# Optimization experiments

Hardware: AMD Instinct MI355X
Metric: run time of the kernel (lower is better)

## Reference

```python
import jax, jax.numpy as jnp
import numpy as np

N, T = 2048, 128
E, H = 128, 256
V, L = 30000, 1000


def setup_inputs() -> dict:
    key = jax.random.key(0)
    ks = jax.random.split(key, 10)
    tokens = jax.random.randint(ks[0], (N, T), 0, V)
    lengths = jax.random.randint(ks[1], (N,), 1, T + 1)  # each seq has >=1 valid step
    labels = jax.random.randint(ks[2], (N,), 0, L)
    s_e = 1.0 / np.sqrt(H)
    emb = jax.random.normal(ks[3], (V, E), dtype=jnp.float32)
    W_ih = jax.random.uniform(ks[4], (4 * H, E), minval=-s_e, maxval=s_e, dtype=jnp.float32)
    W_hh = jax.random.uniform(ks[5], (4 * H, H), minval=-s_e, maxval=s_e, dtype=jnp.float32)
    b_ih = jax.random.uniform(ks[6], (4 * H,), minval=-s_e, maxval=s_e, dtype=jnp.float32)
    b_hh = jax.random.uniform(ks[7], (4 * H,), minval=-s_e, maxval=s_e, dtype=jnp.float32)
    s_h = 1.0 / np.sqrt(H)
    W_out = jax.random.uniform(ks[8], (L, H), minval=-s_h, maxval=s_h, dtype=jnp.float32)
    b_out = jax.random.uniform(ks[9], (L,), minval=-s_h, maxval=s_h, dtype=jnp.float32)
    return {"tokens": tokens, "lengths": lengths, "labels": labels, "emb": emb,
            "W_ih": W_ih, "W_hh": W_hh, "b_ih": b_ih, "b_hh": b_hh,
            "W_out": W_out, "b_out": b_out}


def _lstm_final(tokens, lengths, emb, W_ih, W_hh, b_ih, b_hh):
    # Batched ragged LSTM: freeze state once t >= length (matches per-seq loop).
    x = emb[tokens]                                    # [N,T,E]
    xg = jnp.einsum('nte,ge->ntg', x, W_ih) + b_ih     # [N,T,4H] precomputed input gates
    xg_t = jnp.transpose(xg, (1, 0, 2))                # [T,N,4H]
    mask_t = (jnp.arange(T)[:, None] < lengths[None, :])  # [T,N]
    h0 = jnp.zeros((tokens.shape[0], H), jnp.float32)
    c0 = jnp.zeros_like(h0)

    def step(carry, inp):
        h, c = carry
        xgt, m = inp
        gates = xgt + h @ W_hh.T + b_hh                # [N,4H]
        i, f, g, o = jnp.split(gates, 4, axis=-1)
        i = jax.nn.sigmoid(i); f = jax.nn.sigmoid(f)
        g = jnp.tanh(g); o = jax.nn.sigmoid(o)
        c_new = f * c + i * g
        h_new = o * jnp.tanh(c_new)
        mm = m[:, None]
        return (jnp.where(mm, h_new, h), jnp.where(mm, c_new, c)), None

    (h_f, c_f), _ = jax.lax.scan(step, (h0, c0), (xg_t, mask_t))
    return h_f, c_f                                    # final valid h, c per sequence


def reference(tokens, lengths, labels, emb, W_ih, W_hh, b_ih, b_hh, W_out, b_out):
    h_f, c_f = _lstm_final(tokens, lengths, emb, W_ih, W_hh, b_ih, b_hh)
    logits = h_f @ W_out.T + b_out                     # [N,L]
    logp = jax.nn.log_softmax(logits, axis=-1)
    # NLLLoss per sequence, summed then divided by count -> mean
    loss = -jnp.mean(logp[jnp.arange(logp.shape[0]), labels])
    embeds = jnp.mean(c_f, axis=0)                     # mean of final cell states, [H]
    return embeds, loss
```

## Files before the change

### kernel.cpp

```cpp
#include <hip/hip_runtime.h>
#include <hip/hip_bf16.h>
#include <math.h>

#define NSEQ 2048
#define TT   128
#define EE   128
#define HH   256
#define GG   1024
#define LL   1000
#define NT   512
#define NGRP 32
#define NMEM 8
#define SEQG 64
#define NKT  12
#define NMT  64
#define NKT_O 8
#define WSA_ELEMS (NMT * NKT * 64 * 8)
#define WSO_ELEMS (NMT * NKT_O * 64 * 8)
#define GHF_SHORTS ((size_t)NGRP * NMEM * 2 * 4 * 64 * 8)

typedef __attribute__((ext_vector_type(8))) short bf16x8;
typedef __attribute__((ext_vector_type(4))) float f32x4;
typedef unsigned long long u64;

__device__ __forceinline__ unsigned short f2bf(float f) {
    union { float f; unsigned u; } v; v.f = f;
    unsigned r = v.u + 0x7FFF + ((v.u >> 16) & 1);
    return (unsigned short)(r >> 16);
}
__device__ __forceinline__ float sigf(float x) { return 1.0f / (1.0f + __expf(-x)); }
__device__ __forceinline__ float tanh_fast(float x) { return 1.0f - 2.0f / (1.0f + __expf(2.0f * x)); }

__device__ __forceinline__ void st8_sys(unsigned short* p, unsigned lo, unsigned hi) {
    u64 v = (u64)lo | ((u64)hi << 32);
    __hip_atomic_store((u64*)p, v, __ATOMIC_RELAXED, __HIP_MEMORY_SCOPE_SYSTEM);
}
__device__ __forceinline__ bf16x8 ld16_sys(const unsigned short* p) {
    u64 lo = __hip_atomic_load((const u64*)p,       __ATOMIC_RELAXED, __HIP_MEMORY_SCOPE_SYSTEM);
    u64 hi = __hip_atomic_load((const u64*)(p + 4), __ATOMIC_RELAXED, __HIP_MEMORY_SCOPE_SYSTEM);
    union { u64 q[2]; bf16x8 v; } u; u.q[0] = lo; u.q[1] = hi;
    return u.v;
}

__global__ void init_out_kernel(float* out, int* flags) {
    int i = blockIdx.x * blockDim.x + threadIdx.x;
    if (i < HH + 1) out[i] = 0.0f;
    if (i < NGRP * NMEM) flags[i] = 0;
}

__global__ void convert_weights(const float* __restrict__ Wih, const float* __restrict__ Whh,
                                const float* __restrict__ Wout,
                                unsigned short* __restrict__ wsA, unsigned short* __restrict__ wsO) {
    int gid = blockIdx.x * blockDim.x + threadIdx.x;
    if (gid < NMT * NKT * 64) {
        int lane = gid & 63, tile = gid >> 6;
        int kt = tile % NKT, mt = tile / NKT;
        int row = mt * 16 + (lane & 15);
        int kb  = kt * 32 + (lane >> 4) * 8;
        unsigned short o[8];
#pragma unroll
        for (int j = 0; j < 8; ++j) {
            int k = kb + j;
            float v = (k < EE) ? Wih[row * EE + k] : Whh[row * HH + (k - EE)];
            o[j] = f2bf(v);
        }
        uint4 pk;
        pk.x = o[0] | ((unsigned)o[1] << 16); pk.y = o[2] | ((unsigned)o[3] << 16);
        pk.z = o[4] | ((unsigned)o[5] << 16); pk.w = o[6] | ((unsigned)o[7] << 16);
        *(uint4*)(wsA + (size_t)gid * 8) = pk;
    } else {
        int g2 = gid - NMT * NKT * 64;
        if (g2 < NMT * NKT_O * 64) {
            int lane = g2 & 63, tile = g2 >> 6;
            int kt = tile % NKT_O, mt = tile / NKT_O;
            int row = mt * 16 + (lane & 15);
            int ub  = kt * 32 + (lane >> 4) * 8;
            unsigned short o[8];
#pragma unroll
            for (int j = 0; j < 8; ++j)
                o[j] = (row < LL) ? f2bf(Wout[row * HH + ub + j]) : (unsigned short)0;
            uint4 pk;
            pk.x = o[0] | ((unsigned)o[1] << 16); pk.y = o[2] | ((unsigned)o[3] << 16);
            pk.z = o[4] | ((unsigned)o[5] << 16); pk.w = o[6] | ((unsigned)o[7] << 16);
            *(uint4*)(wsO + (size_t)g2 * 8) = pk;
        }
    }
}

__launch_bounds__(NT, 2)
__global__ void lstm_group_kernel(
    const int* __restrict__ tokens, const int* __restrict__ lengths,
    const int* __restrict__ labels, const float* __restrict__ emb,
    const float* __restrict__ bih,  const float* __restrict__ bhh,
    const float* __restrict__ bout,
    const unsigned short* __restrict__ wsA, const unsigned short* __restrict__ wsO,
    unsigned short* __restrict__ ghf, int* __restrict__ flags,
    float* __restrict__ out)
{
    __shared__ __align__(16) unsigned short wlds[8 * 12 * 64 * 8];
    __shared__ __align__(16) unsigned short xf[2 * 4 * 4 * 64 * 8];
    __shared__ __align__(16) unsigned short hf[2 * 4 * 64 * 8];
    __shared__ float bias_s[128];
    __shared__ int   labv[SEQG];
    __shared__ int   ready_s;

    const int tid = threadIdx.x;
    const int w   = tid >> 6;
    const int l   = tid & 63;
    const int lq  = l >> 4;
    const int ls  = l & 15;
    const int jj  = w >> 2;
    const int cg  = w & 3;
    const int grp = blockIdx.x & (NGRP - 1);
    const int m   = blockIdx.x >> 5;
    const int n0  = grp * SEQG;

    int* const flagBase = flags + grp * NMEM;

    int maxlen = lengths[n0 + l];
#pragma unroll
    for (int s = 1; s < 64; s <<= 1) maxlen = max(maxlen, __shfl_xor(maxlen, s, 64));
    const int len_s = lengths[n0 + cg * 16 + ls];

    if (tid < SEQG) labv[tid] = labels[n0 + tid];
    if (tid < 128) {
        int g = tid >> 5, u = tid & 31;
        int row = 256 * g + 32 * m + u;
        bias_s[tid] = bih[row] + bhh[row];
    }
    if (tid == 0) ready_s = 0;

    for (int idx = tid; idx < 8 * 12 * 64; idx += NT) {
        int mtl = idx / 768;
        int rem = idx - mtl * 768;
        int kt = rem >> 6, l2 = rem & 63;
        int g = mtl >> 1, j2 = mtl & 1;
        int gmt = 16 * g + 2 * m + j2;
        *(uint4*)&wlds[(size_t)idx * 8] =
            *(const uint4*)(wsA + ((size_t)(gmt * NKT + kt) * 64 + l2) * 8);
    }

    if (tid < 256) {
        uint4 z = {0, 0, 0, 0};
        *(uint4*)&hf[(size_t)tid * 8] = z;
        size_t base = ((size_t)((grp * NMEM + m) * 2 + 0) * 4) * 512 + (size_t)tid * 8;
        st8_sys(&ghf[base], 0, 0);
        st8_sys(&ghf[base + 4], 0, 0);
    }

    const int xs_s   = tid & 63;
    const int xs_oct = tid >> 6;

    {
        int tok = tokens[(n0 + xs_s) * TT + 0];
        const float* er = emb + (size_t)tok * EE + 16 * xs_oct;
#pragma unroll
        for (int dc = 0; dc < 4; ++dc) {
            f32x4 xv = *(const f32x4*)(er + 4 * dc);
            int d0 = 16 * xs_oct + 4 * dc;
            int kt = d0 >> 5, cgs = xs_s >> 4;
            int lanep = (xs_s & 15) + 16 * ((d0 >> 3) & 3);
            uint2 pk;
            pk.x = f2bf(xv[0]) | ((unsigned)f2bf(xv[1]) << 16);
            pk.y = f2bf(xv[2]) | ((unsigned)f2bf(xv[3]) << 16);
            *(uint2*)&xf[(size_t)(((0 * 4 + kt) * 4 + cgs) * 64 + lanep) * 8 + (d0 & 4)] = pk;
        }
    }
    __syncthreads();
    if (tid == 0)
        __hip_atomic_store(&flagBase[m], 1, __ATOMIC_RELAXED, __HIP_MEMORY_SCOPE_SYSTEM);

    auto relay_wait = [&](int need) {
        if (w == 0) {
            int f;
            do {
                f = 0x7fffffff;
                if (l < NMEM)
                    f = __hip_atomic_load(&flagBase[l], __ATOMIC_RELAXED, __HIP_MEMORY_SCOPE_SYSTEM);
                f = min(f, __shfl_xor(f, 1, 64));
                f = min(f, __shfl_xor(f, 2, 64));
                f = min(f, __shfl_xor(f, 4, 64));
                f = __shfl(f, 0, 64);
                if (f < need) __builtin_amdgcn_s_sleep(2);
            } while (f < need);
            __hip_atomic_store(&ready_s, need, __ATOMIC_RELEASE, __HIP_MEMORY_SCOPE_WORKGROUP);
        } else {
            while (__hip_atomic_load(&ready_s, __ATOMIC_ACQUIRE, __HIP_MEMORY_SCOPE_WORKGROUP) < need)
                __builtin_amdgcn_s_sleep(1);
        }
    };

    float c_reg[4], h_reg[4];
#pragma unroll
    for (int r = 0; r < 4; ++r) { c_reg[r] = 0.0f; h_reg[r] = 0.0f; }

    const int u8      = 2 * jj + (lq >> 1);
    const int lanep_h = 16 * u8 + ls;
    const int joff_h  = 4 * (lq & 1);
    const size_t gb0  = ((size_t)((grp * NMEM + m) * 2 + 0) * 4 + cg) * 512 + (size_t)lanep_h * 8 + joff_h;
    const size_t gb1  = gb0 + 4 * 512;

    for (int t = 0; t < maxlen; ++t) {
        const int cur = t & 1, nxt = cur ^ 1;

        bf16x8 bx[4];
#pragma unroll
        for (int kt = 0; kt < 4; ++kt)
            bx[kt] = *(const bf16x8*)&xf[(size_t)(((cur * 4 + kt) * 4 + cg) * 64 + l) * 8];
        const bf16x8 bo = *(const bf16x8*)&hf[(size_t)((cur * 4 + cg) * 64 + l) * 8];

        const bool doX = (t + 1 < maxlen);
        f32x4 xv[4];
        if (doX) {
            int tok = tokens[(n0 + xs_s) * TT + t + 1];
            const float* er = emb + (size_t)tok * EE + 16 * xs_oct;
#pragma unroll
            for (int dc = 0; dc < 4; ++dc) xv[dc] = *(const f32x4*)(er + 4 * dc);
        }

        f32x4 acc[4];
#pragma unroll
        for (int g = 0; g < 4; ++g)
            acc[g] = *(const f32x4*)&bias_s[g * 32 + 16 * jj + 4 * lq];

#pragma unroll
        for (int kt = 0; kt < 4; ++kt)
#pragma unroll
            for (int g = 0; g < 4; ++g)
                acc[g] = __builtin_amdgcn_mfma_f32_16x16x32_bf16(
                    *(const bf16x8*)&wlds[(size_t)(((2 * g + jj) * 12 + kt) * 64 + l) * 8],
                    bx[kt], acc[g], 0, 0, 0);

        relay_wait(t + 1);

        bf16x8 bp[7];
#pragma unroll
        for (int i = 0; i < 7; ++i) {
            int p = i + (i >= m ? 1 : 0);
            size_t b = ((size_t)((grp * NMEM + p) * 2 + cur) * 4 + cg) * 512;
            bp[i] = ld16_sys(&ghf[b + (size_t)l * 8]);
        }

#pragma unroll
        for (int g = 0; g < 4; ++g)
            acc[g] = __builtin_amdgcn_mfma_f32_16x16x32_bf16(
                *(const bf16x8*)&wlds[(size_t)(((2 * g + jj) * 12 + 4 + m) * 64 + l) * 8],
                bo, acc[g], 0, 0, 0);
#pragma unroll
        for (int i = 0; i < 7; ++i) {
            int p = i + (i >= m ? 1 : 0);
            int kt = 4 + p;
#pragma unroll
            for (int g = 0; g < 4; ++g)
                acc[g] = __builtin_amdgcn_mfma_f32_16x16x32_bf16(
                    *(const bf16x8*)&wlds[(size_t)(((2 * g + jj) * 12 + kt) * 64 + l) * 8],
                    bp[i], acc[g], 0, 0, 0);
        }

        const bool live = (t < len_s);
#pragma unroll
        for (int r = 0; r < 4; ++r) {
            if (live) {
                float ig = sigf(acc[0][r]);
                float fg = sigf(acc[1][r]);
                float gg = tanh_fast(acc[2][r]);
                float og = sigf(acc[3][r]);
                float cc = fg * c_reg[r] + ig * gg;
                c_reg[r] = cc;
                h_reg[r] = og * tanh_fast(cc);
            }
        }

        {
            uint2 hp;
            hp.x = f2bf(h_reg[0]) | ((unsigned)f2bf(h_reg[1]) << 16);
            hp.y = f2bf(h_reg[2]) | ((unsigned)f2bf(h_reg[3]) << 16);
            *(uint2*)&hf[(size_t)((nxt * 4 + cg) * 64 + lanep_h) * 8 + joff_h] = hp;
            st8_sys(&ghf[((t + 1) & 1) ? gb1 : gb0], hp.x, hp.y);
        }
        if (doX) {
#pragma unroll
            for (int dc = 0; dc < 4; ++dc) {
                int d0 = 16 * xs_oct + 4 * dc;
                int kt = d0 >> 5, cgs = xs_s >> 4;
                int lanep = (xs_s & 15) + 16 * ((d0 >> 3) & 3);
                uint2 pk;
                pk.x = f2bf(xv[dc][0]) | ((unsigned)f2bf(xv[dc][1]) << 16);
                pk.y = f2bf(xv[dc][2]) | ((unsigned)f2bf(xv[dc][3]) << 16);
                *(uint2*)&xf[(size_t)(((nxt * 4 + kt) * 4 + cgs) * 64 + lanep) * 8 + (d0 & 4)] = pk;
            }
        }

        __syncthreads();
        if (tid == 0)
            __hip_atomic_store(&flagBase[m], t + 2, __ATOMIC_RELAXED, __HIP_MEMORY_SCOPE_SYSTEM);
    }

#pragma unroll
    for (int r = 0; r < 4; ++r) {
        float v = c_reg[r];
        v += __shfl_xor(v, 1, 64);
        v += __shfl_xor(v, 2, 64);
        v += __shfl_xor(v, 4, 64);
        v += __shfl_xor(v, 8, 64);
        if (ls == 0)
            atomicAdd(&out[32 * m + 16 * jj + 4 * lq + r], v * (1.0f / NSEQ));
    }

    if (m == 0) {
        relay_wait(maxlen + 1);
        const int fin = maxlen & 1;
        float* lg = (float*)wlds;
        float lossAcc = 0.0f;

        for (int cgo = 0; cgo < 4; ++cgo) {
            bf16x8 bq[8];
#pragma unroll
            for (int p = 0; p < 8; ++p) {
                size_t b = ((size_t)((grp * NMEM + p) * 2 + fin) * 4 + cgo) * 512;
                bq[p] = ld16_sys(&ghf[b + (size_t)l * 8]);
            }
            __syncthreads();
#pragma unroll
            for (int i = 0; i < 8; ++i) {
                int mt = 8 * w + i;
                f32x4 a = {0.0f, 0.0f, 0.0f, 0.0f};
#pragma unroll
                for (int p = 0; p < 8; ++p)
                    a = __builtin_amdgcn_mfma_f32_16x16x32_bf16(
                        *(const bf16x8*)(wsO + ((size_t)(mt * NKT_O + p) * 64 + l) * 8),
                        bq[p], a, 0, 0, 0);
#pragma unroll
                for (int r = 0; r < 4; ++r) {
                    int cls = 16 * mt + 4 * lq + r;
                    lg[(size_t)ls * 1024 + cls] = (cls < LL) ? (a[r] + bout[cls]) : -INFINITY;
                }
            }
            __syncthreads();
            const int s2 = tid >> 5;
            const int i2 = tid & 31;
            const float* row = &lg[(size_t)s2 * 1024];
            float mx = -INFINITY;
#pragma unroll
            for (int k = 0; k < 32; ++k) mx = fmaxf(mx, row[i2 + 32 * k]);
            mx = fmaxf(mx, __shfl_xor(mx, 1, 64));
            mx = fmaxf(mx, __shfl_xor(mx, 2, 64));
            mx = fmaxf(mx, __shfl_xor(mx, 4, 64));
            mx = fmaxf(mx, __shfl_xor(mx, 8, 64));
            mx = fmaxf(mx, __shfl_xor(mx, 16, 64));
            float sm = 0.0f;
#pragma unroll
            for (int k = 0; k < 32; ++k) sm += __expf(row[i2 + 32 * k] - mx);
            sm += __shfl_xor(sm, 1, 64);
            sm += __shfl_xor(sm, 2, 64);
            sm += __shfl_xor(sm, 4, 64);
            sm += __shfl_xor(sm, 8, 64);
            sm += __shfl_xor(sm, 16, 64);
            if (i2 == 0) {
                int lab = labv[cgo * 16 + s2];
                float lp = row[lab] - mx - __logf(sm);
                lossAcc += -lp;
            }
        }
        if ((tid & 31) == 0)
            atomicAdd(&out[HH], lossAcc * (1.0f / NSEQ));
    }
}

extern "C" void kernel_launch(void* const* d_in, const int* in_sizes, int n_in,
                              void* d_out, int out_size, void* d_ws, size_t ws_size,
                              hipStream_t stream)
{
    const int*   tokens  = (const int*)d_in[0];
    const int*   lengths = (const int*)d_in[1];
    const int*   labels  = (const int*)d_in[2];
    const float* emb     = (const float*)d_in[3];
    const float* Wih     = (const float*)d_in[4];
    const float* Whh     = (const float*)d_in[5];
    const float* bih     = (const float*)d_in[6];
    const float* bhh     = (const float*)d_in[7];
    const float* Wout    = (const float*)d_in[8];
    const float* bout    = (const float*)d_in[9];
    float* out = (float*)d_out;

    unsigned short* wsA  = (unsigned short*)d_ws;
    unsigned short* wsO  = wsA + WSA_ELEMS;
    unsigned short* ghf  = wsO + WSO_ELEMS;
    int*            flg  = (int*)(ghf + GHF_SHORTS);

    hipLaunchKernelGGL(init_out_kernel, dim3(1), dim3(512), 0, stream, out, flg);
    {
        int nthr = NMT * NKT * 64 + NMT * NKT_O * 64;
        hipLaunchKernelGGL(convert_weights, dim3((nthr + 255) / 256), dim3(256), 0, stream,
                           Wih, Whh, Wout, wsA, wsO);
    }
    hipLaunchKernelGGL(lstm_group_kernel, dim3(NGRP * NMEM), dim3(NT), 0, stream,
                       tokens, lengths, labels, emb, bih, bhh, bout, wsA, wsO, ghf, flg, out);
}
```

Measured before the change: 708.8 us.

## Software-pipeline input-gate MFMAs one step ahead and keep bias in registers

Computes the input-projection MFMAs for step t+1 into a separate accumulator while waiting for the cross-block relay at step t. The embedding gather moves two steps ahead, and the x staging buffer is reduced to a single buffer. Bias values now live in registers instead of LDS. This takes the input-gate MFMAs off the critical path after the relay wait, at the cost of an extra __syncthreads per step and more register pressure (accN, prefetched xv).

```diff
diff --git a/kernel.cpp b/kernel.cpp
--- a/kernel.cpp
+++ b/kernel.cpp
@@ -98,9 +98,10 @@
     float* __restrict__ out)
 {
     __shared__ __align__(16) unsigned short wlds[8 * 12 * 64 * 8];
-    __shared__ __align__(16) unsigned short xf[2 * 4 * 4 * 64 * 8];
+    __shared__ __align__(16) unsigned short xfS[4 * 4 * 64 * 8];
     __shared__ __align__(16) unsigned short hf[2 * 4 * 64 * 8];
-    __shared__ float bias_s[128];
+    __shared__ float redm[8][16];
+    __shared__ float reds[8][16];
     __shared__ int   labv[SEQG];
     __shared__ int   ready_s;
 
@@ -123,12 +124,16 @@
     const int len_s = lengths[n0 + cg * 16 + ls];
 
     if (tid < SEQG) labv[tid] = labels[n0 + tid];
-    if (tid < 128) {
-        int g = tid >> 5, u = tid & 31;
-        int row = 256 * g + 32 * m + u;
-        bias_s[tid] = bih[row] + bhh[row];
-    }
     if (tid == 0) ready_s = 0;
+
+    f32x4 biasv[4];
+#pragma unroll
+    for (int g = 0; g < 4; ++g)
+#pragma unroll
+        for (int r = 0; r < 4; ++r) {
+            int row = 256 * g + 32 * m + 16 * jj + 4 * lq + r;
+            biasv[g][r] = bih[row] + bhh[row];
+        }
 
     for (int idx = tid; idx < 8 * 12 * 64; idx += NT) {
         int mtl = idx / 768;
@@ -151,24 +156,52 @@
     const int xs_s   = tid & 63;
     const int xs_oct = tid >> 6;
 
-    {
-        int tok = tokens[(n0 + xs_s) * TT + 0];
-        const float* er = emb + (size_t)tok * EE + 16 * xs_oct;
+    auto stageX = [&](const f32x4* xv) {
 #pragma unroll
         for (int dc = 0; dc < 4; ++dc) {
-            f32x4 xv = *(const f32x4*)(er + 4 * dc);
             int d0 = 16 * xs_oct + 4 * dc;
             int kt = d0 >> 5, cgs = xs_s >> 4;
             int lanep = (xs_s & 15) + 16 * ((d0 >> 3) & 3);
             uint2 pk;
-            pk.x = f2bf(xv[0]) | ((unsigned)f2bf(xv[1]) << 16);
-            pk.y = f2bf(xv[2]) | ((unsigned)f2bf(xv[3]) << 16);
-            *(uint2*)&xf[(size_t)(((0 * 4 + kt) * 4 + cgs) * 64 + lanep) * 8 + (d0 & 4)] = pk;
-        }
+            pk.x = f2bf(xv[dc][0]) | ((unsigned)f2bf(xv[dc][1]) << 16);
+            pk.y = f2bf(xv[dc][2]) | ((unsigned)f2bf(xv[dc][3]) << 16);
+            *(uint2*)&xfS[(size_t)((kt * 4 + cgs) * 64 + lanep) * 8 + (d0 & 4)] = pk;
+        }
+    };
+
+    {
+        int tok = tokens[(n0 + xs_s) * TT + 0];
+        const float* er = emb + (size_t)tok * EE + 16 * xs_oct;
+        f32x4 x0[4];
+#pragma unroll
+        for (int dc = 0; dc < 4; ++dc) x0[dc] = *(const f32x4*)(er + 4 * dc);
+        stageX(x0);
     }
     __syncthreads();
     if (tid == 0)
         __hip_atomic_store(&flagBase[m], 1, __ATOMIC_RELAXED, __HIP_MEMORY_SCOPE_SYSTEM);
+
+    f32x4 xv[4];
+    if (maxlen > 1) {
+        int tok = tokens[(n0 + xs_s) * TT + 1];
+        const float* er = emb + (size_t)tok * EE + 16 * xs_oct;
+#pragma unroll
+        for (int dc = 0; dc < 4; ++dc) xv[dc] = *(const f32x4*)(er + 4 * dc);
+    }
+
+    f32x4 acc[4], accN[4];
+#pragma unroll
+    for (int g = 0; g < 4; ++g) acc[g] = biasv[g];
+#pragma unroll
+    for (int kt = 0; kt < 4; ++kt) {
+        const bf16x8 bx = *(const bf16x8*)&xfS[(size_t)((kt * 4 + cg) * 64 + l) * 8];
+#pragma unroll
+        for (int g = 0; g < 4; ++g)
+            acc[g] = __builtin_amdgcn_mfma_f32_16x16x32_bf16(
+                *(const bf16x8*)&wlds[(size_t)(((2 * g + jj) * 12 + kt) * 64 + l) * 8],
+                bx, acc[g], 0, 0, 0);
+    }
+    __syncthreads();
 
     auto relay_wait = [&](int need) {
         if (w == 0) {
@@ -202,34 +235,32 @@
 
     for (int t = 0; t < maxlen; ++t) {
         const int cur = t & 1, nxt = cur ^ 1;
-
-        bf16x8 bx[4];
-#pragma unroll
-        for (int kt = 0; kt < 4; ++kt)
-            bx[kt] = *(const bf16x8*)&xf[(size_t)(((cur * 4 + kt) * 4 + cg) * 64 + l) * 8];
+        const bool doX = (t + 1 < maxlen);
+
+        if (doX) stageX(xv);
         const bf16x8 bo = *(const bf16x8*)&hf[(size_t)((cur * 4 + cg) * 64 + l) * 8];
-
-        const bool doX = (t + 1 < maxlen);
-        f32x4 xv[4];
+        if (doX) __syncthreads();
+
+        if (t + 2 < maxlen) {
+            int tok = tokens[(n0 + xs_s) * TT + t + 2];
+            const float* er = emb + (size_t)tok * EE + 16 * xs_oct;
+#pragma unroll
+            for (int dc = 0; dc < 4; ++dc) xv[dc] = *(const f32x4*)(er + 4 * dc);
+        }
+
         if (doX) {
-            int tok = tokens[(n0 + xs_s) * TT + t + 1];
-            const float* er = emb + (size_t)tok * EE + 16 * xs_oct;
-#pragma unroll
-            for (int dc = 0; dc < 4; ++dc) xv[dc] = *(const f32x4*)(er + 4 * dc);
-        }
-
-        f32x4 acc[4];
-#pragma unroll
-        for (int g = 0; g < 4; ++g)
-            acc[g] = *(const f32x4*)&bias_s[g * 32 + 16 * jj + 4 * lq];
-
-#pragma unroll
-        for (int kt = 0; kt < 4; ++kt)
-#pragma unroll
-            for (int g = 0; g < 4; ++g)
-                acc[g] = __builtin_amdgcn_mfma_f32_16x16x32_bf16(
-                    *(const bf16x8*)&wlds[(size_t)(((2 * g + jj) * 12 + kt) * 64 + l) * 8],
-                    bx[kt], acc[g], 0, 0, 0);
+#pragma unroll
+            for (int g = 0; g < 4; ++g) accN[g] = biasv[g];
+#pragma unroll
+            for (int kt = 0; kt < 4; ++kt) {
+                const bf16x8 bx = *(const bf16x8*)&xfS[(size_t)((kt * 4 + cg) * 64 + l) * 8];
+#pragma unroll
+                for (int g = 0; g < 4; ++g)
+                    accN[g] = __builtin_amdgcn_mfma_f32_16x16x32_bf16(
+                        *(const bf16x8*)&wlds[(size_t)(((2 * g + jj) * 12 + kt) * 64 + l) * 8],
+                        bx, accN[g], 0, 0, 0);
+            }
+        }
 
         relay_wait(t + 1);
 
@@ -271,24 +302,17 @@
             }
         }
 
+        if (doX) {
+#pragma unroll
+            for (int g = 0; g < 4; ++g) acc[g] = accN[g];
+        }
+
         {
             uint2 hp;
             hp.x = f2bf(h_reg[0]) | ((unsigned)f2bf(h_reg[1]) << 16);
             hp.y = f2bf(h_reg[2]) | ((unsigned)f2bf(h_reg[3]) << 16);
             *(uint2*)&hf[(size_t)((nxt * 4 + cg) * 64 + lanep_h) * 8 + joff_h] = hp;
             st8_sys(&ghf[((t + 1) & 1) ? gb1 : gb0], hp.x, hp.y);
-        }
-        if (doX) {
-#pragma unroll
-            for (int dc = 0; dc < 4; ++dc) {
-                int d0 = 16 * xs_oct + 4 * dc;
-                int kt = d0 >> 5, cgs = xs_s >> 4;
-                int lanep = (xs_s & 15) + 16 * ((d0 >> 3) & 3);
-                uint2 pk;
-                pk.x = f2bf(xv[dc][0]) | ((unsigned)f2bf(xv[dc][1]) << 16);
-                pk.y = f2bf(xv[dc][2]) | ((unsigned)f2bf(xv[dc][3]) << 16);
-                *(uint2*)&xf[(size_t)(((nxt * 4 + kt) * 4 + cgs) * 64 + lanep) * 8 + (d0 & 4)] = pk;
-            }
         }
 
         __syncthreads();
```

Result: no change. 700.7 us (-1.1%).

## Replace block-wide barriers with per-wave flag synchronization in LSTM recurrence

Applied to the files above, without the earlier changes.

Removes the per-step __syncthreads and the LDS relay from wave 0. Each wave now publishes its own flag and polls only the 16 producer flags it depends on, and it reads all eight h slices from global memory, including its own block's. The embedding load and the input-gate MFMAs for step t+1 are issued right after the flag store, so they overlap the wait. This cuts barrier and relay latency on the serial critical path. The cost is more global polling traffic, eight times as many flags, and a tighter reliance on the memory-ordering behaviour of relaxed system-scope atomics.

```diff
diff --git a/kernel.cpp b/kernel.cpp
--- a/kernel.cpp
+++ b/kernel.cpp
@@ -18,6 +18,7 @@
 #define WSA_ELEMS (NMT * NKT * 64 * 8)
 #define WSO_ELEMS (NMT * NKT_O * 64 * 8)
 #define GHF_SHORTS ((size_t)NGRP * NMEM * 2 * 4 * 64 * 8)
+#define NFLAGS (NGRP * NMEM * 4 * 2)
 
 typedef __attribute__((ext_vector_type(8))) short bf16x8;
 typedef __attribute__((ext_vector_type(4))) float f32x4;
@@ -45,7 +46,7 @@
 __global__ void init_out_kernel(float* out, int* flags) {
     int i = blockIdx.x * blockDim.x + threadIdx.x;
     if (i < HH + 1) out[i] = 0.0f;
-    if (i < NGRP * NMEM) flags[i] = 0;
+    if (i < NFLAGS) flags[i] = 0;
 }
 
 __global__ void convert_weights(const float* __restrict__ Wih, const float* __restrict__ Whh,
@@ -88,7 +89,7 @@
 }
 
 __launch_bounds__(NT, 2)
-__global__ void lstm_group_kernel(
+__global__ void lstm_wave_kernel(
     const int* __restrict__ tokens, const int* __restrict__ lengths,
     const int* __restrict__ labels, const float* __restrict__ emb,
     const float* __restrict__ bih,  const float* __restrict__ bhh,
@@ -98,11 +99,7 @@
     float* __restrict__ out)
 {
     __shared__ __align__(16) unsigned short wlds[8 * 12 * 64 * 8];
-    __shared__ __align__(16) unsigned short xf[2 * 4 * 4 * 64 * 8];
-    __shared__ __align__(16) unsigned short hf[2 * 4 * 64 * 8];
-    __shared__ float bias_s[128];
-    __shared__ int   labv[SEQG];
-    __shared__ int   ready_s;
+    __shared__ int labv[SEQG];
 
     const int tid = threadIdx.x;
     const int w   = tid >> 6;
@@ -115,20 +112,24 @@
     const int m   = blockIdx.x >> 5;
     const int n0  = grp * SEQG;
 
-    int* const flagBase = flags + grp * NMEM;
+    int* const flagBase = flags + grp * (NMEM * 8);
 
     int maxlen = lengths[n0 + l];
 #pragma unroll
     for (int s = 1; s < 64; s <<= 1) maxlen = max(maxlen, __shfl_xor(maxlen, s, 64));
     const int len_s = lengths[n0 + cg * 16 + ls];
+    const int myseq = n0 + cg * 16 + ls;
 
     if (tid < SEQG) labv[tid] = labels[n0 + tid];
-    if (tid < 128) {
-        int g = tid >> 5, u = tid & 31;
-        int row = 256 * g + 32 * m + u;
-        bias_s[tid] = bih[row] + bhh[row];
-    }
-    if (tid == 0) ready_s = 0;
+
+    f32x4 biasv[4];
+#pragma unroll
+    for (int g = 0; g < 4; ++g)
+#pragma unroll
+        for (int r = 0; r < 4; ++r) {
+            int row = 256 * g + 32 * m + 16 * jj + 4 * lq + r;
+            biasv[g][r] = bih[row] + bhh[row];
+        }
 
     for (int idx = tid; idx < 8 * 12 * 64; idx += NT) {
         int mtl = idx / 768;
@@ -140,122 +141,88 @@
             *(const uint4*)(wsA + ((size_t)(gmt * NKT + kt) * 64 + l2) * 8);
     }
 
-    if (tid < 256) {
-        uint4 z = {0, 0, 0, 0};
-        *(uint4*)&hf[(size_t)tid * 8] = z;
-        size_t base = ((size_t)((grp * NMEM + m) * 2 + 0) * 4) * 512 + (size_t)tid * 8;
-        st8_sys(&ghf[base], 0, 0);
-        st8_sys(&ghf[base + 4], 0, 0);
-    }
-
-    const int xs_s   = tid & 63;
-    const int xs_oct = tid >> 6;
-
-    {
-        int tok = tokens[(n0 + xs_s) * TT + 0];
-        const float* er = emb + (size_t)tok * EE + 16 * xs_oct;
-#pragma unroll
-        for (int dc = 0; dc < 4; ++dc) {
-            f32x4 xv = *(const f32x4*)(er + 4 * dc);
-            int d0 = 16 * xs_oct + 4 * dc;
-            int kt = d0 >> 5, cgs = xs_s >> 4;
-            int lanep = (xs_s & 15) + 16 * ((d0 >> 3) & 3);
-            uint2 pk;
-            pk.x = f2bf(xv[0]) | ((unsigned)f2bf(xv[1]) << 16);
-            pk.y = f2bf(xv[2]) | ((unsigned)f2bf(xv[3]) << 16);
-            *(uint2*)&xf[(size_t)(((0 * 4 + kt) * 4 + cgs) * 64 + lanep) * 8 + (d0 & 4)] = pk;
-        }
-    }
-    __syncthreads();
-    if (tid == 0)
-        __hip_atomic_store(&flagBase[m], 1, __ATOMIC_RELAXED, __HIP_MEMORY_SCOPE_SYSTEM);
-
-    auto relay_wait = [&](int need) {
-        if (w == 0) {
-            int f;
-            do {
-                f = 0x7fffffff;
-                if (l < NMEM)
-                    f = __hip_atomic_load(&flagBase[l], __ATOMIC_RELAXED, __HIP_MEMORY_SCOPE_SYSTEM);
-                f = min(f, __shfl_xor(f, 1, 64));
-                f = min(f, __shfl_xor(f, 2, 64));
-                f = min(f, __shfl_xor(f, 4, 64));
-                f = __shfl(f, 0, 64);
-                if (f < need) __builtin_amdgcn_s_sleep(2);
-            } while (f < need);
-            __hip_atomic_store(&ready_s, need, __ATOMIC_RELEASE, __HIP_MEMORY_SCOPE_WORKGROUP);
-        } else {
-            while (__hip_atomic_load(&ready_s, __ATOMIC_ACQUIRE, __HIP_MEMORY_SCOPE_WORKGROUP) < need)
-                __builtin_amdgcn_s_sleep(1);
-        }
-    };
-
-    float c_reg[4], h_reg[4];
-#pragma unroll
-    for (int r = 0; r < 4; ++r) { c_reg[r] = 0.0f; h_reg[r] = 0.0f; }
-
     const int u8      = 2 * jj + (lq >> 1);
     const int lanep_h = 16 * u8 + ls;
     const int joff_h  = 4 * (lq & 1);
     const size_t gb0  = ((size_t)((grp * NMEM + m) * 2 + 0) * 4 + cg) * 512 + (size_t)lanep_h * 8 + joff_h;
     const size_t gb1  = gb0 + 4 * 512;
+    const int myFlag  = m * 8 + cg * 2 + jj;
+
+    st8_sys(&ghf[gb0], 0, 0);
+
+    const int xoff = (l >> 4) * 8;
+    bf16x8 bx[4];
+    {
+        int tok = tokens[myseq * TT + 0];
+        const float* er = emb + (size_t)tok * EE + xoff;
+#pragma unroll
+        for (int kt = 0; kt < 4; ++kt) {
+            f32x4 a = *(const f32x4*)(er + kt * 32);
+            f32x4 b = *(const f32x4*)(er + kt * 32 + 4);
+            union { unsigned u[4]; bf16x8 v; } pk;
+            pk.u[0] = f2bf(a[0]) | ((unsigned)f2bf(a[1]) << 16);
+            pk.u[1] = f2bf(a[2]) | ((unsigned)f2bf(a[3]) << 16);
+            pk.u[2] = f2bf(b[0]) | ((unsigned)f2bf(b[1]) << 16);
+            pk.u[3] = f2bf(b[2]) | ((unsigned)f2bf(b[3]) << 16);
+            bx[kt] = pk.v;
+        }
+    }
+
+    __syncthreads();
+
+    __builtin_amdgcn_s_waitcnt(0);
+    asm volatile("" ::: "memory");
+    if (l == 0)
+        __hip_atomic_store(&flagBase[myFlag], 1, __ATOMIC_RELAXED, __HIP_MEMORY_SCOPE_SYSTEM);
+
+    f32x4 acc[4];
+#pragma unroll
+    for (int g = 0; g < 4; ++g) acc[g] = biasv[g];
+#pragma unroll
+    for (int kt = 0; kt < 4; ++kt)
+#pragma unroll
+        for (int g = 0; g < 4; ++g)
+            acc[g] = __builtin_amdgcn_mfma_f32_16x16x32_bf16(
+                *(const bf16x8*)&wlds[(size_t)(((2 * g + jj) * 12 + kt) * 64 + l) * 8],
+                bx[kt], acc[g], 0, 0, 0);
+
+    float c_reg[4], h_reg[4];
+#pragma unroll
+    for (int r = 0; r < 4; ++r) { c_reg[r] = 0.0f; h_reg[r] = 0.0f; }
+
+    auto wave_wait = [&](int need) {
+        int f;
+        do {
+            f = 0x7fffffff;
+            if (l < 16)
+                f = __hip_atomic_load(&flagBase[(l >> 1) * 8 + cg * 2 + (l & 1)],
+                                      __ATOMIC_RELAXED, __HIP_MEMORY_SCOPE_SYSTEM);
+            f = min(f, __shfl_xor(f, 1, 64));
+            f = min(f, __shfl_xor(f, 2, 64));
+            f = min(f, __shfl_xor(f, 4, 64));
+            f = min(f, __shfl_xor(f, 8, 64));
+            f = __shfl(f, 0, 64);
+        } while (f < need);
+    };
 
     for (int t = 0; t < maxlen; ++t) {
-        const int cur = t & 1, nxt = cur ^ 1;
-
-        bf16x8 bx[4];
-#pragma unroll
-        for (int kt = 0; kt < 4; ++kt)
-            bx[kt] = *(const bf16x8*)&xf[(size_t)(((cur * 4 + kt) * 4 + cg) * 64 + l) * 8];
-        const bf16x8 bo = *(const bf16x8*)&hf[(size_t)((cur * 4 + cg) * 64 + l) * 8];
-
-        const bool doX = (t + 1 < maxlen);
-        f32x4 xv[4];
-        if (doX) {
-            int tok = tokens[(n0 + xs_s) * TT + t + 1];
-            const float* er = emb + (size_t)tok * EE + 16 * xs_oct;
-#pragma unroll
-            for (int dc = 0; dc < 4; ++dc) xv[dc] = *(const f32x4*)(er + 4 * dc);
-        }
-
-        f32x4 acc[4];
-#pragma unroll
-        for (int g = 0; g < 4; ++g)
-            acc[g] = *(const f32x4*)&bias_s[g * 32 + 16 * jj + 4 * lq];
-
-#pragma unroll
-        for (int kt = 0; kt < 4; ++kt)
+        const int par = t & 1;
+
+        wave_wait(t + 1);
+
+        bf16x8 bp[8];
+#pragma unroll
+        for (int p = 0; p < 8; ++p) {
+            size_t b = ((size_t)((grp * NMEM + p) * 2 + par) * 4 + cg) * 512;
+            bp[p] = ld16_sys(&ghf[b + (size_t)l * 8]);
+        }
+#pragma unroll
+        for (int p = 0; p < 8; ++p)
 #pragma unroll
             for (int g = 0; g < 4; ++g)
                 acc[g] = __builtin_amdgcn_mfma_f32_16x16x32_bf16(
-                    *(const bf16x8*)&wlds[(size_t)(((2 * g + jj) * 12 + kt) * 64 + l) * 8],
-                    bx[kt], acc[g], 0, 0, 0);
-
-        relay_wait(t + 1);
-
-        bf16x8 bp[7];
-#pragma unroll
-        for (int i = 0; i < 7; ++i) {
-            int p = i + (i >= m ? 1 : 0);
-            size_t b = ((size_t)((grp * NMEM + p) * 2 + cur) * 4 + cg) * 512;
-            bp[i] = ld16_sys(&ghf[b + (size_t)l * 8]);
-        }
-
-#pragma unroll
-        for (int g = 0; g < 4; ++g)
-            acc[g] = __builtin_amdgcn_mfma_f32_16x16x32_bf16(
-                *(const bf16x8*)&wlds[(size_t)(((2 * g + jj) * 12 + 4 + m) * 64 + l) * 8],
-                bo, acc[g], 0, 0, 0);
-#pragma unroll
-        for (int i = 0; i < 7; ++i) {
-            int p = i + (i >= m ? 1 : 0);
-            int kt = 4 + p;
-#pragma unroll
-            for (int g = 0; g < 4; ++g)
-                acc[g] = __builtin_amdgcn_mfma_f32_16x16x32_bf16(
-                    *(const bf16x8*)&wlds[(size_t)(((2 * g + jj) * 12 + kt) * 64 + l) * 8],
-                    bp[i], acc[g], 0, 0, 0);
-        }
+                    *(const bf16x8*)&wlds[(size_t)(((2 * g + jj) * 12 + 4 + p) * 64 + l) * 8],
+                    bp[p], acc[g], 0, 0, 0);
 
         const bool live = (t < len_s);
 #pragma unroll
@@ -275,25 +242,37 @@
             uint2 hp;
             hp.x = f2bf(h_reg[0]) | ((unsigned)f2bf(h_reg[1]) << 16);
             hp.y = f2bf(h_reg[2]) | ((unsigned)f2bf(h_reg[3]) << 16);
-            *(uint2*)&hf[(size_t)((nxt * 4 + cg) * 64 + lanep_h) * 8 + joff_h] = hp;
-            st8_sys(&ghf[((t + 1) & 1) ? gb1 : gb0], hp.x, hp.y);
-        }
-        if (doX) {
-#pragma unroll
-            for (int dc = 0; dc < 4; ++dc) {
-                int d0 = 16 * xs_oct + 4 * dc;
-                int kt = d0 >> 5, cgs = xs_s >> 4;
-                int lanep = (xs_s & 15) + 16 * ((d0 >> 3) & 3);
-                uint2 pk;
-                pk.x = f2bf(xv[dc][0]) | ((unsigned)f2bf(xv[dc][1]) << 16);
-                pk.y = f2bf(xv[dc][2]) | ((unsigned)f2bf(xv[dc][3]) << 16);
-                *(uint2*)&xf[(size_t)(((nxt * 4 + kt) * 4 + cgs) * 64 + lanep) * 8 + (d0 & 4)] = pk;
-            }
-        }
-
-        __syncthreads();
-        if (tid == 0)
-            __hip_atomic_store(&flagBase[m], t + 2, __ATOMIC_RELAXED, __HIP_MEMORY_SCOPE_SYSTEM);
+            st8_sys(&ghf[par ? gb0 : gb1], hp.x, hp.y);
+        }
+        __builtin_amdgcn_s_waitcnt(0);
+        asm volatile("" ::: "memory");
+        if (l == 0)
+            __hip_atomic_store(&flagBase[myFlag], t + 2, __ATOMIC_RELAXED, __HIP_MEMORY_SCOPE_SYSTEM);
+
+        if (t + 1 < maxlen) {
+            int tok = tokens[myseq * TT + t + 1];
+            const float* er = emb + (size_t)tok * EE + xoff;
+#pragma unroll
+            for (int kt = 0; kt < 4; ++kt) {
+                f32x4 a = *(const f32x4*)(er + kt * 32);
+                f32x4 b = *(const f32x4*)(er + kt * 32 + 4);
+                union { unsigned u[4]; bf16x8 v; } pk;
+                pk.u[0] = f2bf(a[0]) | ((unsigned)f2bf(a[1]) << 16);
+                pk.u[1] = f2bf(a[2]) | ((unsigned)f2bf(a[3]) << 16);
+                pk.u[2] = f2bf(b[0]) | ((unsigned)f2bf(b[1]) << 16);
+                pk.u[3] = f2bf(b[2]) | ((unsigned)f2bf(b[3]) << 16);
+                bx[kt] = pk.v;
+            }
+#pragma unroll
+            for (int g = 0; g < 4; ++g) acc[g] = biasv[g];
+#pragma unroll
+            for (int kt = 0; kt < 4; ++kt)
+#pragma unroll
+                for (int g = 0; g < 4; ++g)
+                    acc[g] = __builtin_amdgcn_mfma_f32_16x16x32_bf16(
+                        *(const bf16x8*)&wlds[(size_t)(((2 * g + jj) * 12 + kt) * 64 + l) * 8],
+                        bx[kt], acc[g], 0, 0, 0);
+        }
     }
 
 #pragma unroll
@@ -308,7 +287,18 @@
     }
 
     if (m == 0) {
-        relay_wait(maxlen + 1);
+        {
+            int f;
+            do {
+                f = __hip_atomic_load(&flagBase[l], __ATOMIC_RELAXED, __HIP_MEMORY_SCOPE_SYSTEM);
+                f = min(f, __shfl_xor(f, 1, 64));
+                f = min(f, __shfl_xor(f, 2, 64));
+                f = min(f, __shfl_xor(f, 4, 64));
+                f = min(f, __shfl_xor(f, 8, 64));
+                f = min(f, __shfl_xor(f, 16, 64));
+                f = min(f, __shfl_xor(f, 32, 64));
+            } while (f < maxlen + 1);
+        }
         const int fin = maxlen & 1;
         float* lg = (float*)wlds;
         float lossAcc = 0.0f;
@@ -388,12 +378,12 @@
     unsigned short* ghf  = wsO + WSO_ELEMS;
     int*            flg  = (int*)(ghf + GHF_SHORTS);
 
-    hipLaunchKernelGGL(init_out_kernel, dim3(1), dim3(512), 0, stream, out, flg);
+    hipLaunchKernelGGL(init_out_kernel, dim3(8), dim3(512), 0, stream, out, flg);
     {
         int nthr = NMT * NKT * 64 + NMT * NKT_O * 64;
         hipLaunchKernelGGL(convert_weights, dim3((nthr + 255) / 256), dim3(256), 0, stream,
                            Wih, Whh, Wout, wsA, wsO);
     }
-    hipLaunchKernelGGL(lstm_group_kernel, dim3(NGRP * NMEM), dim3(NT), 0, stream,
+    hipLaunchKernelGGL(lstm_wave_kernel, dim3(NGRP * NMEM), dim3(NT), 0, stream,
                        tokens, lengths, labels, emb, bih, bhh, bout, wsA, wsO, ghf, flg, out);
 }
```

Result: slower. 1.442 ms (+103.5%).
